# Performance work log

Measured on AMD Instinct MI355X. Metric: run time of the kernel, lower is better.

## Reference

```python
import jax, jax.numpy as jnp
import numpy as np

N, H2, T = 64, 1024, 512  # num steps/documents, 2*hidden_dim, tokens per step
EPS = 1e-12  # torch F.normalize eps


def setup_inputs() -> dict:
    key = jax.random.key(0)
    k1, k2, k3, k4 = jax.random.split(key, 4)
    return {
        "hidden_states": jax.random.normal(k1, (N, H2, T), dtype=jnp.float32),
        "W_attention": jax.random.normal(k2, (H2, H2), dtype=jnp.float32),
        "bias_attention": jax.random.normal(k3, (H2,), dtype=jnp.float32),
        "u_w0": jax.random.normal(k4, (H2,), dtype=jnp.float32),
    }


def reference(hidden_states, W_attention, bias_attention, u_w0):
    n = hidden_states.shape[0]

    # Sequential recurrence on u_w: u_w <- normalize(u_w @ W^T + b), updated
    # BEFORE being used at each step i. Collect the post-update value per step.
    def step(u, _):
        u_new = u @ W_attention.T + bias_attention
        u_new = u_new / jnp.maximum(jnp.linalg.norm(u_new), EPS)
        return u_new, u_new

    _, u_ws = jax.lax.scan(step, u_w0, None, length=n)  # (N, 2H)

    # u_it = tanh(h_i^T W^T + b) for all steps, batched: (N, T, 2H)
    u_it = jnp.tanh(jnp.einsum('ndt,ed->nte', hidden_states, W_attention)
                    + bias_attention)

    # attention scores per step, softmax over the T axis (torch Softmax(dim=0)
    # on a (T,1) column)
    scores = jnp.einsum('nte,ne->nt', u_it, u_ws)  # (N, T)
    a = jax.nn.softmax(scores, axis=1)

    # weighted sum s_i = h_i @ a_i -> stacked as rows: (N, 2H)
    s = jnp.einsum('ndt,nt->nd', hidden_states, a)
    return s
```

## Files before the change

### kernel.cpp

```cpp
#include <hip/hip_runtime.h>
#include <cstdint>
#include <cstddef>

#define H2 1024
#define TT 512
#define NSTEPS 64
#define RBLK 32
#define RTHR 512

using floatx4 = __attribute__((__ext_vector_type__(4))) float;
using half8   = __attribute__((__ext_vector_type__(8))) _Float16;
using half4   = __attribute__((__ext_vector_type__(4))) _Float16;

__device__ __forceinline__ float tanh_fast(float x) {
  return 1.0f - 2.0f / (__expf(2.0f * x) + 1.0f);
}

#define GLDS16(gp, lp)                                                         \
  __builtin_amdgcn_global_load_lds(                                            \
      (const __attribute__((address_space(1))) void*)(gp),                     \
      (__attribute__((address_space(3))) void*)(lp), 16, 0, 0)

__global__ __launch_bounds__(RTHR, 1) void recur_kernel(
    const float* __restrict__ W, const float* __restrict__ bias,
    const float* __restrict__ u0, float* __restrict__ vbuf,
    float* __restrict__ norm2, unsigned* __restrict__ ctr) {
  __shared__ __align__(16) float ub[H2 + 64];
  __shared__ float bred[8];
  int tid = threadIdx.x;
  int row = tid >> 4, g = tid & 15;
  int r = blockIdx.x * RBLK + row;
  int wv = tid >> 6, lane = tid & 63;

  const float4* wr = (const float4*)(W + ((size_t)r << 10) + (g << 6));
  float bl = bias[r];

  for (int i = 0; i < NSTEPS; ++i) {
    float4 wreg[16];
#pragma unroll
    for (int j = 0; j < 16; ++j) wreg[j] = wr[j];

    if (i > 0) {
      if (tid == 0) {
        unsigned tgt = (unsigned)(RBLK * i);
        while (__hip_atomic_load(ctr, __ATOMIC_RELAXED,
                                 __HIP_MEMORY_SCOPE_AGENT) < tgt)
          __builtin_amdgcn_s_sleep(1);
      }
      __syncthreads();
    }

    float x0, x1;
    if (i == 0) {
      x0 = u0[2 * tid];
      x1 = u0[2 * tid + 1];
    } else {
      float* src = vbuf + ((size_t)(i - 1) << 10);
      x0 = __hip_atomic_load(src + 2 * tid, __ATOMIC_RELAXED,
                             __HIP_MEMORY_SCOPE_AGENT);
      x1 = __hip_atomic_load(src + 2 * tid + 1, __ATOMIC_RELAXED,
                             __HIP_MEMORY_SCOPE_AGENT);
    }
    {
      int f = 2 * tid;
      int addr = f + 4 * (f >> 6);
      float2 v2;
      v2.x = x0;
      v2.y = x1;
      *(float2*)(ub + addr) = v2;
    }
    float sq = x0 * x0 + x1 * x1;
#pragma unroll
    for (int off = 1; off <= 32; off <<= 1) sq += __shfl_xor(sq, off, 64);
    if (lane == 0) bred[wv] = sq;
    __syncthreads();
    float nrm = 0.f;
#pragma unroll
    for (int k2 = 0; k2 < 8; ++k2) nrm += bred[k2];
    float rs = (i == 0) ? 1.0f : 1.0f / fmaxf(sqrtf(nrm), 1e-12f);
    if (i > 0 && blockIdx.x == 0 && tid == 0) norm2[i - 1] = nrm;

    const float4* ug = (const float4*)(ub + 68 * g);
    float acc = 0.f;
#pragma unroll
    for (int j = 0; j < 16; ++j) {
      float4 a = wreg[j], c = ug[j];
      acc += a.x * c.x + a.y * c.y + a.z * c.z + a.w * c.w;
    }
#pragma unroll
    for (int off = 1; off <= 8; off <<= 1) acc += __shfl_xor(acc, off, 64);

    if (g == 0) {
      float v = acc * rs + bl;
      __hip_atomic_store(vbuf + ((size_t)i << 10) + r, v, __ATOMIC_RELAXED,
                         __HIP_MEMORY_SCOPE_AGENT);
    }
    asm volatile("s_waitcnt vmcnt(0)" ::: "memory");
    __syncthreads();
    if (tid == 0)
      __hip_atomic_fetch_add(ctr, 1u, __ATOMIC_RELAXED,
                             __HIP_MEMORY_SCOPE_AGENT);
  }

  if (blockIdx.x == 0) {
    if (tid == 0) {
      while (__hip_atomic_load(ctr, __ATOMIC_RELAXED,
                               __HIP_MEMORY_SCOPE_AGENT) <
             (unsigned)(RBLK * NSTEPS))
        __builtin_amdgcn_s_sleep(1);
    }
    __syncthreads();
    float* src = vbuf + ((size_t)(NSTEPS - 1) << 10);
    float x0 = __hip_atomic_load(src + 2 * tid, __ATOMIC_RELAXED,
                                 __HIP_MEMORY_SCOPE_AGENT);
    float x1 = __hip_atomic_load(src + 2 * tid + 1, __ATOMIC_RELAXED,
                                 __HIP_MEMORY_SCOPE_AGENT);
    float sq = x0 * x0 + x1 * x1;
#pragma unroll
    for (int off = 1; off <= 32; off <<= 1) sq += __shfl_xor(sq, off, 64);
    if (lane == 0) bred[wv] = sq;
    __syncthreads();
    if (tid == 0) {
      float nrm = 0.f;
#pragma unroll
      for (int k2 = 0; k2 < 8; ++k2) nrm += bred[k2];
      norm2[NSTEPS - 1] = nrm;
    }
  }
}

__global__ __launch_bounds__(256) void wconv_kernel(const float* __restrict__ W,
                                                    _Float16* __restrict__ Wh) {
  int i = blockIdx.x * 256 + threadIdx.x;
  float4 v = ((const float4*)W)[i];
  half4 o = {(_Float16)v.x, (_Float16)v.y, (_Float16)v.z, (_Float16)v.w};
  ((half4*)Wh)[i] = o;
}

__global__ __launch_bounds__(256) void transpose_h(const float* __restrict__ h,
                                                   _Float16* __restrict__ hhT) {
  int n = blockIdx.z, d0 = blockIdx.x * 64, t0 = blockIdx.y * 64;
  __shared__ float tile[64][65];
  const float* hb = h + ((size_t)n * H2 + d0) * TT + t0;
  int dr = threadIdx.x >> 4, tc = (threadIdx.x & 15) << 2;
#pragma unroll
  for (int p = 0; p < 4; ++p) {
    float4 v = *(const float4*)(hb + (size_t)(dr + p * 16) * TT + tc);
    tile[dr + p * 16][tc] = v.x;
    tile[dr + p * 16][tc + 1] = v.y;
    tile[dr + p * 16][tc + 2] = v.z;
    tile[dr + p * 16][tc + 3] = v.w;
  }
  __syncthreads();
  _Float16* ob = hhT + ((size_t)n * TT + t0) * H2 + d0;
  int tr = threadIdx.x >> 3, seg = threadIdx.x & 7;
#pragma unroll
  for (int p = 0; p < 2; ++p) {
    int t = tr + p * 32;
    half8 hv;
#pragma unroll
    for (int u = 0; u < 8; ++u) hv[u] = (_Float16)tile[seg * 8 + u][t];
    *(half8*)(ob + (size_t)t * H2 + seg * 8) = hv;
  }
}

__global__ __launch_bounds__(256) void gemm2(
    const _Float16* __restrict__ Wh, const _Float16* __restrict__ hhT,
    const float* __restrict__ bias, const float* __restrict__ vbuf,
    const float* __restrict__ norm2, float* __restrict__ scores) {
  int x = blockIdx.x;
  int xcd = x & 7, slot = x >> 3;
  int e_t = slot & 7;
  int tn = xcd * 32 + (slot >> 3);
  int t_t = tn & 3, n = tn >> 2;
  int e_base = e_t * 128, t_base = t_t * 128;

  int tid = threadIdx.x, lane = tid & 63, w = tid >> 6;
  int q = lane >> 4, m = lane & 15;
  int eoff = (w & 1) * 64, toff = (w >> 1) * 64;

  __shared__ __align__(16) _Float16 Ash[128 * 32];
  __shared__ __align__(16) _Float16 Bsh[128 * 32];

  floatx4 zero = {0.f, 0.f, 0.f, 0.f};
  floatx4 acc[4][4];
#pragma unroll
  for (int i = 0; i < 4; ++i)
#pragma unroll
    for (int j = 0; j < 4; ++j) acc[i][j] = zero;

  int rl = lane >> 2, kseg = lane & 3;
  const _Float16* gA0 =
      Wh + (((size_t)(e_base + w * 32 + rl)) << 10) + kseg * 8;
  const _Float16* gA1 = gA0 + ((size_t)16 << 10);
  const _Float16* gB0 = hhT + ((size_t)n << 19) +
                        (((size_t)(t_base + w * 32 + rl)) << 10) + kseg * 8;
  const _Float16* gB1 = gB0 + ((size_t)16 << 10);
  _Float16* lA0 = Ash + (w * 32) * 32;
  _Float16* lA1 = lA0 + 16 * 32;
  _Float16* lB0 = Bsh + (w * 32) * 32;
  _Float16* lB1 = lB0 + 16 * 32;

  for (int k0 = 0; k0 < H2; k0 += 32) {
    GLDS16(gA0 + k0, lA0);
    GLDS16(gA1 + k0, lA1);
    GLDS16(gB0 + k0, lB0);
    GLDS16(gB1 + k0, lB1);
    __syncthreads();

    half8 af[4], bf[4];
#pragma unroll
    for (int i = 0; i < 4; ++i)
      af[i] = *(const half8*)&Ash[(eoff + i * 16 + m) * 32 + q * 8];
#pragma unroll
    for (int j = 0; j < 4; ++j)
      bf[j] = *(const half8*)&Bsh[(toff + j * 16 + m) * 32 + q * 8];
#pragma unroll
    for (int i = 0; i < 4; ++i)
#pragma unroll
      for (int j = 0; j < 4; ++j)
        acc[i][j] =
            __builtin_amdgcn_mfma_f32_16x16x32_f16(af[i], bf[j], acc[i][j], 0, 0, 0);
    __syncthreads();
  }

  float* uloc = (float*)Ash;
  float* bloc = uloc + 128;
  if (tid < 128) {
    float rsn = 1.0f / fmaxf(sqrtf(norm2[n]), 1e-12f);
    uloc[tid] = vbuf[((size_t)n << 10) + e_base + tid] * rsn;
    bloc[tid] = bias[e_base + tid];
  }
  __syncthreads();

  float part[4] = {0.f, 0.f, 0.f, 0.f};
#pragma unroll
  for (int i = 0; i < 4; ++i) {
#pragma unroll
    for (int reg = 0; reg < 4; ++reg) {
      int el = eoff + i * 16 + q * 4 + reg;
      float ubv = uloc[el];
      float bbv = bloc[el];
#pragma unroll
      for (int j = 0; j < 4; ++j) {
        float y = acc[i][j][reg] + bbv;
        part[j] += tanh_fast(y) * ubv;
      }
    }
  }
#pragma unroll
  for (int j = 0; j < 4; ++j) {
    part[j] += __shfl_xor(part[j], 16, 64);
    part[j] += __shfl_xor(part[j], 32, 64);
    if (lane < 16) {
      int t = t_base + toff + j * 16 + lane;
      atomicAdd(&scores[(size_t)n * TT + t], part[j]);
    }
  }
}

__global__ __launch_bounds__(256) void out_kernel(
    const float* __restrict__ h, const float* __restrict__ scores,
    float* __restrict__ out) {
  int n = blockIdx.y;
  int ds = blockIdx.x;
  int tid = threadIdx.x;
  int w = tid >> 6, lane = tid & 63;

  __shared__ float sa[TT];
  __shared__ float wred[8];

  float s0 = scores[(size_t)n * TT + tid];
  float s1 = scores[(size_t)n * TT + 256 + tid];

  float mx = fmaxf(s0, s1);
#pragma unroll
  for (int off = 32; off >= 1; off >>= 1) mx = fmaxf(mx, __shfl_xor(mx, off, 64));
  if (lane == 0) wred[w] = mx;
  __syncthreads();
  mx = fmaxf(fmaxf(wred[0], wred[1]), fmaxf(wred[2], wred[3]));

  float e0 = __expf(s0 - mx);
  float e1 = __expf(s1 - mx);
  float ssum = e0 + e1;
#pragma unroll
  for (int off = 32; off >= 1; off >>= 1) ssum += __shfl_xor(ssum, off, 64);
  if (lane == 0) wred[4 + w] = ssum;
  __syncthreads();
  ssum = wred[4] + wred[5] + wred[6] + wred[7];
  float inv = 1.0f / ssum;
  sa[tid] = e0 * inv;
  sa[tid + 256] = e1 * inv;
  __syncthreads();

  int d0 = ds * 64 + w * 16;
  const float4* hb = reinterpret_cast<const float4*>(h + (size_t)n * H2 * TT);
#pragma unroll 1
  for (int rr = 0; rr < 16; ++rr) {
    int d = d0 + rr;
    const float4* hr = hb + (size_t)d * (TT / 4);
    float4 a4 = hr[lane];
    float4 b4 = hr[64 + lane];
    int t0 = 4 * lane;
    float acc = a4.x * sa[t0] + a4.y * sa[t0 + 1] + a4.z * sa[t0 + 2] +
                a4.w * sa[t0 + 3] + b4.x * sa[256 + t0] +
                b4.y * sa[256 + t0 + 1] + b4.z * sa[256 + t0 + 2] +
                b4.w * sa[256 + t0 + 3];
#pragma unroll
    for (int off = 1; off <= 32; off <<= 1) acc += __shfl_xor(acc, off, 64);
    if (lane == 0) out[(size_t)n * H2 + d] = acc;
  }
}

extern "C" void kernel_launch(void* const* d_in, const int* in_sizes, int n_in,
                              void* d_out, int out_size, void* d_ws, size_t ws_size,
                              hipStream_t stream) {
  const float* h    = (const float*)d_in[0];
  const float* W    = (const float*)d_in[1];
  const float* bias = (const float*)d_in[2];
  const float* u0   = (const float*)d_in[3];
  float* out = (float*)d_out;

  float* wsf    = (float*)d_ws;
  float* norm2  = wsf;
  float* scores = wsf + 64;
  float* vbuf   = wsf + 64 + NSTEPS * TT;
  unsigned* ctr = (unsigned*)(vbuf + (size_t)NSTEPS * H2);
  float* after_ctr = (float*)(ctr + 16);
  size_t fixed_floats = (size_t)(after_ctr - wsf);
  _Float16* Wh  = (_Float16*)after_ctr;
  _Float16* hhT = Wh + (size_t)H2 * H2;
  size_t need = fixed_floats * 4 + (size_t)H2 * H2 * 2 +
                (size_t)NSTEPS * TT * H2 * 2;
  bool big = ws_size >= need;

  hipMemsetAsync(d_ws, 0, (size_t)(64 + NSTEPS * TT) * sizeof(float), stream);
  hipMemsetAsync(ctr, 0, 16 * sizeof(unsigned), stream);

  {
    const float* Wp = W; const float* bp = bias; const float* up = u0;
    float* vp = vbuf; float* np = norm2; unsigned* cp = ctr;
    void* kargs[] = {&Wp, &bp, &up, &vp, &np, &cp};
    hipLaunchCooperativeKernel((void*)recur_kernel, dim3(RBLK), dim3(RTHR),
                               kargs, 0, stream);
  }

  if (big) {
    wconv_kernel<<<dim3(H2 * H2 / 1024), dim3(256), 0, stream>>>(W, Wh);
    transpose_h<<<dim3(16, 8, 64), dim3(256), 0, stream>>>(h, hhT);
    gemm2<<<dim3(2048), dim3(256), 0, stream>>>(Wh, hhT, bias, vbuf, norm2,
                                                scores);
  } else {
    gemm2<<<dim3(2048), dim3(256), 0, stream>>>(Wh, hhT, bias, vbuf, norm2,
                                                scores);
  }

  out_kernel<<<dim3(16, 64), dim3(256), 0, stream>>>(h, scores, out);

  (void)in_sizes; (void)n_in; (void)out_size; (void)ws_size;
}
```

Before: 535.3 us.

## Replace counter barrier in recurrence with per-wave sentinel polling of data

The sequential u_w recurrence no longer uses a global atomic counter and block-wide barriers. vbuf is pre-filled with a 0xFF sentinel, and each wave polls the previous step's vector directly until no sentinel remains. Each wave now owns 4 rows with W held in registers once rather than reloaded every step, and the norm is reduced within a wave, so shared memory and __syncthreads are removed. The cost is heavier polling traffic (every wave reads the full 4KB vector) and reliance on NaN-pattern sentinels never being produced as real values, plus an extra memset of vbuf.

```diff
diff --git a/kernel.cpp b/kernel.cpp
--- a/kernel.cpp
+++ b/kernel.cpp
@@ -11,6 +11,7 @@
 using floatx4 = __attribute__((__ext_vector_type__(4))) float;
 using half8   = __attribute__((__ext_vector_type__(8))) _Float16;
 using half4   = __attribute__((__ext_vector_type__(4))) _Float16;
+typedef unsigned long long u64;
 
 __device__ __forceinline__ float tanh_fast(float x) {
   return 1.0f - 2.0f / (__expf(2.0f * x) + 1.0f);
@@ -21,111 +22,110 @@
       (const __attribute__((address_space(1))) void*)(gp),                     \
       (__attribute__((address_space(3))) void*)(lp), 16, 0, 0)
 
+__device__ __forceinline__ void poll_z(const float* buf, int l, float z[16]) {
+  const u64* src = (const u64*)buf + 2 * l;
+  for (;;) {
+    u64 v[8];
+#pragma unroll
+    for (int j = 0; j < 4; ++j) {
+#pragma unroll
+      for (int q = 0; q < 2; ++q)
+        v[2 * j + q] = __hip_atomic_load(src + 128 * j + q, __ATOMIC_RELAXED,
+                                         __HIP_MEMORY_SCOPE_AGENT);
+    }
+    bool ok = true;
+#pragma unroll
+    for (int j = 0; j < 8; ++j) ok &= (v[j] != ~0ull);
+    if (__all(ok)) {
+#pragma unroll
+      for (int j = 0; j < 8; ++j) {
+        z[2 * j] = __builtin_bit_cast(float, (unsigned)(v[j] & 0xFFFFFFFFu));
+        z[2 * j + 1] = __builtin_bit_cast(float, (unsigned)(v[j] >> 32));
+      }
+      return;
+    }
+    __builtin_amdgcn_s_sleep(2);
+  }
+}
+
 __global__ __launch_bounds__(RTHR, 1) void recur_kernel(
     const float* __restrict__ W, const float* __restrict__ bias,
     const float* __restrict__ u0, float* __restrict__ vbuf,
-    float* __restrict__ norm2, unsigned* __restrict__ ctr) {
-  __shared__ __align__(16) float ub[H2 + 64];
-  __shared__ float bred[8];
+    float* __restrict__ norm2) {
   int tid = threadIdx.x;
-  int row = tid >> 4, g = tid & 15;
-  int r = blockIdx.x * RBLK + row;
-  int wv = tid >> 6, lane = tid & 63;
-
-  const float4* wr = (const float4*)(W + ((size_t)r << 10) + (g << 6));
-  float bl = bias[r];
-
+  int w = tid >> 6, l = tid & 63;
+  int r0 = blockIdx.x * RBLK + w * 4;
+
+  float4 wreg[4][4];
+  float bl[4];
+#pragma unroll
+  for (int p = 0; p < 4; ++p) {
+    const float* wr = W + ((size_t)(r0 + p) << 10) + 4 * l;
+#pragma unroll
+    for (int j = 0; j < 4; ++j) wreg[p][j] = *(const float4*)(wr + 256 * j);
+    bl[p] = bias[r0 + p];
+  }
+
+  float z[16];
   for (int i = 0; i < NSTEPS; ++i) {
-    float4 wreg[16];
-#pragma unroll
-    for (int j = 0; j < 16; ++j) wreg[j] = wr[j];
-
-    if (i > 0) {
-      if (tid == 0) {
-        unsigned tgt = (unsigned)(RBLK * i);
-        while (__hip_atomic_load(ctr, __ATOMIC_RELAXED,
-                                 __HIP_MEMORY_SCOPE_AGENT) < tgt)
-          __builtin_amdgcn_s_sleep(1);
+    if (i == 0) {
+      const float* u = u0 + 4 * l;
+#pragma unroll
+      for (int j = 0; j < 4; ++j)
+#pragma unroll
+        for (int c = 0; c < 4; ++c) z[4 * j + c] = u[256 * j + c];
+    } else {
+      poll_z(vbuf + ((size_t)(i - 1) << 10), l, z);
+    }
+
+    float sq = 0.f;
+#pragma unroll
+    for (int j = 0; j < 16; ++j) sq += z[j] * z[j];
+#pragma unroll
+    for (int off = 1; off <= 32; off <<= 1) sq += __shfl_xor(sq, off, 64);
+    float rs = (i == 0) ? 1.0f : 1.0f / fmaxf(sqrtf(sq), 1e-12f);
+    if (i > 0 && blockIdx.x == 0 && tid == 0) norm2[i - 1] = sq;
+
+    float acc[4];
+#pragma unroll
+    for (int p = 0; p < 4; ++p) {
+      float a = 0.f;
+#pragma unroll
+      for (int j = 0; j < 4; ++j) {
+        float4 wv = wreg[p][j];
+        a += wv.x * z[4 * j] + wv.y * z[4 * j + 1] + wv.z * z[4 * j + 2] +
+             wv.w * z[4 * j + 3];
       }
-      __syncthreads();
-    }
-
-    float x0, x1;
-    if (i == 0) {
-      x0 = u0[2 * tid];
-      x1 = u0[2 * tid + 1];
-    } else {
-      float* src = vbuf + ((size_t)(i - 1) << 10);
-      x0 = __hip_atomic_load(src + 2 * tid, __ATOMIC_RELAXED,
-                             __HIP_MEMORY_SCOPE_AGENT);
-      x1 = __hip_atomic_load(src + 2 * tid + 1, __ATOMIC_RELAXED,
-                             __HIP_MEMORY_SCOPE_AGENT);
-    }
-    {
-      int f = 2 * tid;
-      int addr = f + 4 * (f >> 6);
-      float2 v2;
-      v2.x = x0;
-      v2.y = x1;
-      *(float2*)(ub + addr) = v2;
-    }
-    float sq = x0 * x0 + x1 * x1;
+      acc[p] = a;
+    }
+#pragma unroll
+    for (int p = 0; p < 4; ++p)
+#pragma unroll
+      for (int off = 1; off <= 32; off <<= 1)
+        acc[p] += __shfl_xor(acc[p], off, 64);
+
+    if (l == 0) {
+      float y0 = acc[0] * rs + bl[0], y1 = acc[1] * rs + bl[1];
+      float y2 = acc[2] * rs + bl[2], y3 = acc[3] * rs + bl[3];
+      u64 a01 = ((u64)__builtin_bit_cast(unsigned, y1) << 32) |
+                (u64)__builtin_bit_cast(unsigned, y0);
+      u64 a23 = ((u64)__builtin_bit_cast(unsigned, y3) << 32) |
+                (u64)__builtin_bit_cast(unsigned, y2);
+      u64* dst = (u64*)(vbuf + ((size_t)i << 10) + r0);
+      __hip_atomic_store(dst, a01, __ATOMIC_RELAXED, __HIP_MEMORY_SCOPE_AGENT);
+      __hip_atomic_store(dst + 1, a23, __ATOMIC_RELAXED,
+                         __HIP_MEMORY_SCOPE_AGENT);
+    }
+  }
+
+  if (blockIdx.x == 0 && w == 0) {
+    poll_z(vbuf + ((size_t)(NSTEPS - 1) << 10), l, z);
+    float sq = 0.f;
+#pragma unroll
+    for (int j = 0; j < 16; ++j) sq += z[j] * z[j];
 #pragma unroll
     for (int off = 1; off <= 32; off <<= 1) sq += __shfl_xor(sq, off, 64);
-    if (lane == 0) bred[wv] = sq;
-    __syncthreads();
-    float nrm = 0.f;
-#pragma unroll
-    for (int k2 = 0; k2 < 8; ++k2) nrm += bred[k2];
-    float rs = (i == 0) ? 1.0f : 1.0f / fmaxf(sqrtf(nrm), 1e-12f);
-    if (i > 0 && blockIdx.x == 0 && tid == 0) norm2[i - 1] = nrm;
-
-    const float4* ug = (const float4*)(ub + 68 * g);
-    float acc = 0.f;
-#pragma unroll
-    for (int j = 0; j < 16; ++j) {
-      float4 a = wreg[j], c = ug[j];
-      acc += a.x * c.x + a.y * c.y + a.z * c.z + a.w * c.w;
-    }
-#pragma unroll
-    for (int off = 1; off <= 8; off <<= 1) acc += __shfl_xor(acc, off, 64);
-
-    if (g == 0) {
-      float v = acc * rs + bl;
-      __hip_atomic_store(vbuf + ((size_t)i << 10) + r, v, __ATOMIC_RELAXED,
-                         __HIP_MEMORY_SCOPE_AGENT);
-    }
-    asm volatile("s_waitcnt vmcnt(0)" ::: "memory");
-    __syncthreads();
-    if (tid == 0)
-      __hip_atomic_fetch_add(ctr, 1u, __ATOMIC_RELAXED,
-                             __HIP_MEMORY_SCOPE_AGENT);
-  }
-
-  if (blockIdx.x == 0) {
-    if (tid == 0) {
-      while (__hip_atomic_load(ctr, __ATOMIC_RELAXED,
-                               __HIP_MEMORY_SCOPE_AGENT) <
-             (unsigned)(RBLK * NSTEPS))
-        __builtin_amdgcn_s_sleep(1);
-    }
-    __syncthreads();
-    float* src = vbuf + ((size_t)(NSTEPS - 1) << 10);
-    float x0 = __hip_atomic_load(src + 2 * tid, __ATOMIC_RELAXED,
-                                 __HIP_MEMORY_SCOPE_AGENT);
-    float x1 = __hip_atomic_load(src + 2 * tid + 1, __ATOMIC_RELAXED,
-                                 __HIP_MEMORY_SCOPE_AGENT);
-    float sq = x0 * x0 + x1 * x1;
-#pragma unroll
-    for (int off = 1; off <= 32; off <<= 1) sq += __shfl_xor(sq, off, 64);
-    if (lane == 0) bred[wv] = sq;
-    __syncthreads();
-    if (tid == 0) {
-      float nrm = 0.f;
-#pragma unroll
-      for (int k2 = 0; k2 < 8; ++k2) nrm += bred[k2];
-      norm2[NSTEPS - 1] = nrm;
-    }
+    if (l == 0) norm2[NSTEPS - 1] = sq;
   }
 }
 
@@ -335,12 +335,12 @@
   bool big = ws_size >= need;
 
   hipMemsetAsync(d_ws, 0, (size_t)(64 + NSTEPS * TT) * sizeof(float), stream);
-  hipMemsetAsync(ctr, 0, 16 * sizeof(unsigned), stream);
+  hipMemsetAsync(vbuf, 0xFF, (size_t)NSTEPS * H2 * sizeof(float), stream);
 
   {
     const float* Wp = W; const float* bp = bias; const float* up = u0;
-    float* vp = vbuf; float* np = norm2; unsigned* cp = ctr;
-    void* kargs[] = {&Wp, &bp, &up, &vp, &np, &cp};
+    float* vp = vbuf; float* np = norm2;
+    void* kargs[] = {&Wp, &bp, &up, &vp, &np};
     hipLaunchCooperativeKernel((void*)recur_kernel, dim3(RBLK), dim3(RTHR),
                                kargs, 0, stream);
   }
```

After: 705.7 us. 31.8% more time.
